# Optimization experiments

Hardware: AMD Instinct MI355X
Metric: run time of the kernel (lower is better)

## Reference

```python
import jax, jax.numpy as jnp
import numpy as np

N, L, M, NNZ, P, G, H = 4096, 64, 256, 100000, 3, 1, 8
D = M // H  # head_dim = 32


def setup_inputs() -> dict:
    key = jax.random.key(0)
    ks = jax.random.split(key, 8)
    return {
        "sparse_values": jax.random.normal(ks[0], (NNZ, M), jnp.float32),
        "linear_index": jax.random.randint(ks[1], (N, L), 0, NNZ, jnp.int32),
        "is_specified": jax.random.randint(ks[2], (N, L), 0, 2, jnp.int32).astype(bool),
        "query": jax.random.normal(ks[3], (N, M), jnp.float32),
        "key_weight": jax.random.normal(ks[4], (M, M), jnp.float32) * 0.05,
        "value_weight": jax.random.normal(ks[5], (M, M), jnp.float32) * 0.05,
        "key_positions": jax.random.uniform(ks[6], (N, L, P), jnp.float32),
        "rope_freqs": jax.random.normal(ks[7], (P, G, H, D // 2), jnp.float32),
        "n_heads": H,
    }


def reference(sparse_values, linear_index, is_specified, query, key_weight,
              value_weight, key_positions, rope_freqs, n_heads):
    n, l = linear_index.shape
    m = query.shape[-1]
    h = n_heads
    d = m // h
    scale = 1.0 / np.sqrt(m)  # docstring: default scale_factor = 1/sqrt(M)

    # Gather each query's key subset; unspecified keys -> 0 (will be masked)
    safe_idx = jnp.where(is_specified, linear_index, 0)
    gathered = jnp.where(is_specified[..., None], sparse_values[safe_idx], 0.0)  # [N,L,M]

    # Key / value projections (nn.Linear convention: x @ W.T)
    k = (gathered @ key_weight.T).reshape(n, l, h, d)
    v = (gathered @ value_weight.T).reshape(n, l, h, d)

    # RoPE on keys: angles [N,L,H,D/2], summed over position dims P and freq groups G
    angles = jnp.einsum('nlp,pghd->nlhd', key_positions, rope_freqs)
    cos, sin = jnp.cos(angles), jnp.sin(angles)
    k_even, k_odd = k[..., 0::2], k[..., 1::2]
    k = jnp.stack([k_even * cos - k_odd * sin,
                   k_even * sin + k_odd * cos], axis=-1).reshape(n, l, h, d)

    # Per-query subset attention (query is pre-rotated per docstring)
    q = query.reshape(n, h, d)
    scores = jnp.einsum('nhd,nlhd->nhl', q, k) * scale
    scores = jnp.where(is_specified[:, None, :], scores, -jnp.inf)

    # Queries with all keys unspecified -> zero output (avoid NaN from all -inf)
    any_spec = is_specified.any(axis=-1)  # [N]
    attn = jax.nn.softmax(jnp.where(any_spec[:, None, None], scores, 0.0), axis=-1)
    out = jnp.einsum('nhl,nlhd->nhd', attn, v).reshape(n, m)
    out = jnp.where(any_spec[:, None], out, 0.0)
    return out, is_specified
```

## Files before the change

### kernel.cpp

```cpp
#include <hip/hip_runtime.h>
#include <math.h>

#define N_Q 4096
#define L_K 64
#define M_D 256

typedef float f32x16 __attribute__((ext_vector_type(16)));
typedef __bf16 b16x8 __attribute__((ext_vector_type(8)));
union F8 { uint4 u; unsigned short s[8]; b16x8 v; };

__device__ __forceinline__ unsigned short f2bf(float x) {
  unsigned u = __float_as_uint(x);
  return (unsigned short)((u + 0x7fffu + ((u >> 16) & 1u)) >> 16);
}

__global__ __launch_bounds__(256) void k_prep(const unsigned char* __restrict__ raw,
                                              float* __restrict__ out2,
                                              const float* __restrict__ wv,
                                              float* __restrict__ wvt,
                                              const float* __restrict__ wk,
                                              unsigned short* __restrict__ wkf,
                                              const int* __restrict__ lin,
                                              int* __restrict__ pcnt,
                                              int* __restrict__ plin,
                                              unsigned char* __restrict__ pl) {
  __shared__ int pll_s[256];
  __shared__ unsigned char pls_s[256];
  __shared__ int pc_s[4];
  const int tid = threadIdx.x, lane = tid & 63;
  pll_s[tid] = 0;
  pls_s[tid] = 0;
  int v = 0;
  for (int i = tid; i < 4096; i += 256)
    if (i & 3) v |= raw[i];
  int f = __syncthreads_or(v);
  const int gi = blockIdx.x * 256 + tid;
  bool b = f ? (raw[gi] != 0) : (((const int*)raw)[gi] != 0);
  out2[gi] = b ? 1.0f : 0.0f;
  int li = lin[gi];
  unsigned long long mask = __ballot(b);
  if (b) {
    int rank = __popcll(mask & ((1ull << lane) - 1));
    pll_s[(tid & 192) + rank] = li;
    pls_s[(tid & 192) + rank] = (unsigned char)lane;
  }
  if (lane == 0) pc_s[tid >> 6] = __popcll(mask);
  __syncthreads();
  plin[gi] = pll_s[tid];
  pl[gi] = pls_s[tid];
  if (tid < 4) pcnt[blockIdx.x * 4 + tid] = pc_s[tid];

  if (gi < 65536) {
    wvt[(gi & 255) * 256 + (gi >> 8)] = wv[gi];
    int oc = gi >> 8, k = gi & 255;
    int tt = oc >> 5, c32o = oc & 31;
    int ks = k >> 4, kg2 = (k >> 3) & 1, j = k & 7;
    wkf[(((tt * 16 + ks) << 6) + kg2 * 32 + c32o) * 8 + j] = f2bf(wk[gi]);
  }
}

#define SC_OFF  32768
#define AT_OFF  (SC_OFF + 2048)
#define LDS_SZ  (AT_OFF + 2048)

__global__ __launch_bounds__(256, 4) void k_fused3(
    const float* __restrict__ sv, const float* __restrict__ q,
    const unsigned short* __restrict__ wkf, const float* __restrict__ pos,
    const float* __restrict__ freqs, const int* __restrict__ pcnt,
    const int* __restrict__ plin, const unsigned char* __restrict__ pl,
    unsigned short* __restrict__ agg) {
  __shared__ __align__(16) char smem[LDS_SZ];
  float* sc_s   = (float*)(smem + SC_OFF);
  float* attn_s = (float*)(smem + AT_OFF);
  const int tid = threadIdx.x, lane = tid & 63, w = tid >> 6;
  const int c32 = lane & 31, kg = lane >> 5;
  const int rt = w >> 1, ch = w & 1;
  const int n = blockIdx.x;
  const int cnt = pcnt[n];

  if (cnt == 0) {
    *(uint4*)((char*)agg + (size_t)n * 4096 + tid * 16) = uint4{0, 0, 0, 0};
    return;
  }
  const int ct32 = (cnt + 31) & ~31;
  const int ntiles = ct32 >> 5;

  {
    const int r0 = tid >> 5, ii = tid & 31;
    #pragma unroll
    for (int pp = 0; pp < 8; ++pp) {
      const int rloc = pp * 8 + r0;
      if (rloc < ct32) {
        const int pe = (rloc < cnt) ? rloc : (cnt - 1);
        const float* rp = sv + (size_t)plin[n * 64 + pe] * 256 + ii * 8;
        float4 f0 = *(const float4*)rp;
        float4 f1 = *(const float4*)(rp + 4);
        F8 pk;
        pk.s[0] = f2bf(f0.x); pk.s[1] = f2bf(f0.y); pk.s[2] = f2bf(f0.z); pk.s[3] = f2bf(f0.w);
        pk.s[4] = f2bf(f1.x); pk.s[5] = f2bf(f1.y); pk.s[6] = f2bf(f1.z); pk.s[7] = f2bf(f1.w);
        *(uint4*)(smem + rloc * 512 + ((ii ^ (rloc & 31)) << 4)) = pk.u;
      }
    }
  }

  const int p = rt * 32 + c32;
  const bool pv = p < cnt;
  const int pe2 = pv ? p : (cnt - 1);
  const int l = pl[n * 64 + pe2];
  const float* lp = pos + ((size_t)n * 64 + l) * 3;
  const float pp0 = lp[0], pp1 = lp[1], pp2 = lp[2];

  __syncthreads();

  if (rt < ntiles) {
    f32x16 acc[4];
    #pragma unroll
    for (int t = 0; t < 4; ++t)
      #pragma unroll
      for (int r = 0; r < 16; ++r) acc[t][r] = 0.0f;

    const char* fbase = (const char*)wkf + ch * 65536 + lane * 16;
    F8 afc[4], afn[4];
    #pragma unroll
    for (int t = 0; t < 4; ++t) afc[t].u = *(const uint4*)(fbase + (t * 16) * 1024);

    #pragma unroll
    for (int ks = 0; ks < 16; ++ks) {
      if (ks < 15) {
        #pragma unroll
        for (int t = 0; t < 4; ++t)
          afn[t].u = *(const uint4*)(fbase + (t * 16 + ks + 1) * 1024);
      }
      F8 bf;
      bf.u = *(const uint4*)(smem + (rt * 32 + c32) * 512 + ((((ks << 1) + kg) ^ c32) << 4));
      #pragma unroll
      for (int t = 0; t < 4; ++t)
        acc[t] = __builtin_amdgcn_mfma_f32_32x32x16_bf16(afc[t].v, bf.v, acc[t], 0, 0, 0);
      #pragma unroll
      for (int t = 0; t < 4; ++t) afc[t] = afn[t];
    }

    #pragma unroll
    for (int t = 0; t < 4; ++t) {
      const int h = ch * 4 + t;
      const float* qh = q + (size_t)n * 256 + h * 32;
      const float* F = freqs + h * 16;
      float s = 0.f;
      #pragma unroll
      for (int g = 0; g < 4; ++g) {
        #pragma unroll
        for (int pr = 0; pr < 2; ++pr) {
          const int d0 = g * 8 + kg * 4 + pr * 2;
          const int jj = d0 >> 1;
          const int r = g * 4 + pr * 2;
          float ke = acc[t][r], ko = acc[t][r + 1];
          float ang = pp0 * F[jj] + pp1 * F[128 + jj] + pp2 * F[256 + jj];
          float sn = __sinf(ang), cs = __cosf(ang);
          float2 qq = *(const float2*)(qh + d0);
          s += ke * (cs * qq.x + sn * qq.y) + ko * (cs * qq.y - sn * qq.x);
        }
      }
      s += __shfl_xor(s, 32);
      if (kg == 0 && pv) sc_s[p * 8 + h] = s * 0.0625f;
    }
  }
  __syncthreads();

  #pragma unroll
  for (int uu = 0; uu < 2; ++uu) {
    const int h = w * 2 + uu;
    const bool vl = lane < cnt;
    float v = vl ? sc_s[lane * 8 + h] : -__builtin_inff();
    float mx = v;
    #pragma unroll
    for (int o = 32; o; o >>= 1) mx = fmaxf(mx, __shfl_xor(mx, o));
    float e = vl ? __expf(v - mx) : 0.f;
    float sm = e;
    #pragma unroll
    for (int o = 32; o; o >>= 1) sm += __shfl_xor(sm, o);
    if (vl) attn_s[lane * 8 + h] = e / sm;
  }
  __syncthreads();

  const int m = tid;
  float ga[8];
  #pragma unroll
  for (int h = 0; h < 8; ++h) ga[h] = 0.f;
  #pragma unroll 4
  for (int p2 = 0; p2 < cnt; ++p2) {
    unsigned short us = *(const unsigned short*)(smem + p2 * 512 +
                        ((((m >> 3) ^ (p2 & 31)) << 4) | ((m & 7) << 1)));
    float gv = __uint_as_float((unsigned)us << 16);
    const float4* ap = (const float4*)(attn_s + p2 * 8);
    float4 aA = ap[0], aB = ap[1];
    ga[0] += aA.x * gv; ga[1] += aA.y * gv; ga[2] += aA.z * gv; ga[3] += aA.w * gv;
    ga[4] += aB.x * gv; ga[5] += aB.y * gv; ga[6] += aB.z * gv; ga[7] += aB.w * gv;
  }
  #pragma unroll
  for (int h = 0; h < 8; ++h)
    agg[(size_t)n * 2048 + h * 256 + m] = f2bf(ga[h]);
}

__global__ __launch_bounds__(256) void k_out(const unsigned short* __restrict__ agg,
                                             const float* __restrict__ wvt,
                                             float* __restrict__ out) {
  __shared__ float a_s[4][8][260];
  const int tid = threadIdx.x;
  const int n0 = blockIdx.x * 4;
  #pragma unroll
  for (int it = 0; it < 4; ++it) {
    uint4 v = *(const uint4*)(agg + (size_t)(n0 + it) * 2048 + tid * 8);
    const unsigned short* sp = (const unsigned short*)&v;
    const int hh = tid >> 5, m0 = (tid & 31) * 8;
    #pragma unroll
    for (int k2 = 0; k2 < 8; ++k2)
      a_s[it][hh][m0 + k2] = __uint_as_float((unsigned)sp[k2] << 16);
  }
  __syncthreads();
  const int m = tid, h = m >> 5;
  float o0 = 0.f, o1 = 0.f, o2 = 0.f, o3 = 0.f;
  #pragma unroll 8
  for (int j = 0; j < 256; ++j) {
    float wvv = wvt[j * 256 + m];
    o0 += a_s[0][h][j] * wvv;
    o1 += a_s[1][h][j] * wvv;
    o2 += a_s[2][h][j] * wvv;
    o3 += a_s[3][h][j] * wvv;
  }
  out[(n0 + 0) * 256 + m] = o0;
  out[(n0 + 1) * 256 + m] = o1;
  out[(n0 + 2) * 256 + m] = o2;
  out[(n0 + 3) * 256 + m] = o3;
}

extern "C" void kernel_launch(void* const* d_in, const int* in_sizes, int n_in,
                              void* d_out, int out_size, void* d_ws, size_t ws_size,
                              hipStream_t stream) {
  const float* sv  = (const float*)d_in[0];
  const int* lin   = (const int*)d_in[1];
  const unsigned char* raw = (const unsigned char*)d_in[2];
  const float* q   = (const float*)d_in[3];
  const float* wk  = (const float*)d_in[4];
  const float* wv  = (const float*)d_in[5];
  const float* pos = (const float*)d_in[6];
  const float* fq  = (const float*)d_in[7];
  float* out = (float*)d_out;
  char* ws = (char*)d_ws;

  float* wvt          = (float*)ws;
  unsigned short* wkf = (unsigned short*)(ws + 262144);
  int* pcnt           = (int*)(ws + 393216);
  int* plin           = (int*)(ws + 409600);
  unsigned char* pl   = (unsigned char*)(ws + 1458176);
  unsigned short* agg = (unsigned short*)(ws + 1720320);

  k_prep  <<<1024, 256, 0, stream>>>(raw, out + N_Q * M_D, wv, wvt, wk, wkf,
                                     lin, pcnt, plin, pl);
  k_fused3<<<4096, 256, 0, stream>>>(sv, q, wkf, pos, fq, pcnt, plin, pl, agg);
  k_out   <<<1024, 256, 0, stream>>>(agg, wvt, out);
}
```

Measured before the change: 107.8 us.

## Pre-convert sparse table to bf16 and double-buffer async row gathers into LDS

Adds a kernel that converts the entire sparse_values table to bf16, then gathers rows from that image directly into LDS via global_load_lds. Each block now processes four queries, prefetching the next query's rows into a second LDS buffer while computing the current one, and the XOR swizzle is replaced with a padded row stride. The aim is to hide gather latency and halve gather bytes, at the cost of a full-table conversion pass each call and lower occupancy.

```diff
diff --git a/kernel.cpp b/kernel.cpp
--- a/kernel.cpp
+++ b/kernel.cpp
@@ -4,6 +4,7 @@
 #define N_Q 4096
 #define L_K 64
 #define M_D 256
+#define NNZ_ROWS 100000
 
 typedef float f32x16 __attribute__((ext_vector_type(16)));
 typedef __bf16 b16x8 __attribute__((ext_vector_type(8)));
@@ -12,6 +13,19 @@
 __device__ __forceinline__ unsigned short f2bf(float x) {
   unsigned u = __float_as_uint(x);
   return (unsigned short)((u + 0x7fffu + ((u >> 16) & 1u)) >> 16);
+}
+
+__global__ __launch_bounds__(256) void k_img(const float* __restrict__ sv,
+                                             unsigned short* __restrict__ img) {
+  const int s = blockIdx.x * 256 + threadIdx.x;
+  const int r = s >> 5, k0 = (s & 31) << 3;
+  const float* rp = sv + (size_t)r * 256 + k0;
+  float4 f0 = *(const float4*)rp;
+  float4 f1 = *(const float4*)(rp + 4);
+  F8 pk;
+  pk.s[0] = f2bf(f0.x); pk.s[1] = f2bf(f0.y); pk.s[2] = f2bf(f0.z); pk.s[3] = f2bf(f0.w);
+  pk.s[4] = f2bf(f1.x); pk.s[5] = f2bf(f1.y); pk.s[6] = f2bf(f1.z); pk.s[7] = f2bf(f1.w);
+  *(uint4*)(img + (size_t)r * 256 + k0) = pk.u;
 }
 
 __global__ __launch_bounds__(256) void k_prep(const unsigned char* __restrict__ raw,
@@ -59,146 +73,155 @@
   }
 }
 
-#define SC_OFF  32768
-#define AT_OFF  (SC_OFF + 2048)
-#define LDS_SZ  (AT_OFF + 2048)
-
-__global__ __launch_bounds__(256, 4) void k_fused3(
-    const float* __restrict__ sv, const float* __restrict__ q,
+#define GSTRIDE 560
+#define BUF_SZ  (64 * GSTRIDE)
+#define SC_OFF  (2 * BUF_SZ)
+#define LDS_SZ  (SC_OFF + 2048)
+
+__global__ __launch_bounds__(256, 2) void k_fused5(
+    const unsigned short* __restrict__ img, const float* __restrict__ q,
     const unsigned short* __restrict__ wkf, const float* __restrict__ pos,
     const float* __restrict__ freqs, const int* __restrict__ pcnt,
     const int* __restrict__ plin, const unsigned char* __restrict__ pl,
     unsigned short* __restrict__ agg) {
   __shared__ __align__(16) char smem[LDS_SZ];
-  float* sc_s   = (float*)(smem + SC_OFF);
-  float* attn_s = (float*)(smem + AT_OFF);
+  float* sc_s = (float*)(smem + SC_OFF);
   const int tid = threadIdx.x, lane = tid & 63, w = tid >> 6;
   const int c32 = lane & 31, kg = lane >> 5;
   const int rt = w >> 1, ch = w & 1;
-  const int n = blockIdx.x;
-  const int cnt = pcnt[n];
-
-  if (cnt == 0) {
-    *(uint4*)((char*)agg + (size_t)n * 4096 + tid * 16) = uint4{0, 0, 0, 0};
-    return;
-  }
-  const int ct32 = (cnt + 31) & ~31;
-  const int ntiles = ct32 >> 5;
-
-  {
-    const int r0 = tid >> 5, ii = tid & 31;
-    #pragma unroll
-    for (int pp = 0; pp < 8; ++pp) {
-      const int rloc = pp * 8 + r0;
-      if (rloc < ct32) {
-        const int pe = (rloc < cnt) ? rloc : (cnt - 1);
-        const float* rp = sv + (size_t)plin[n * 64 + pe] * 256 + ii * 8;
-        float4 f0 = *(const float4*)rp;
-        float4 f1 = *(const float4*)(rp + 4);
-        F8 pk;
-        pk.s[0] = f2bf(f0.x); pk.s[1] = f2bf(f0.y); pk.s[2] = f2bf(f0.z); pk.s[3] = f2bf(f0.w);
-        pk.s[4] = f2bf(f1.x); pk.s[5] = f2bf(f1.y); pk.s[6] = f2bf(f1.z); pk.s[7] = f2bf(f1.w);
-        *(uint4*)(smem + rloc * 512 + ((ii ^ (rloc & 31)) << 4)) = pk.u;
+  const int n_base = blockIdx.x * 4;
+
+  auto stage = [&](int n, char* buf, int cn) {
+    #pragma unroll
+    for (int j = 0; j < 16; ++j) {
+      const int r = w * 16 + j;
+      if (r < cn) {
+        const int pv = plin[n * 64 + r];
+        const unsigned int* src =
+            (const unsigned int*)((const char*)img + (size_t)pv * 512);
+        __builtin_amdgcn_global_load_lds(
+            (const __attribute__((address_space(1))) unsigned int*)(src + lane),
+            (__attribute__((address_space(3))) unsigned int*)(buf + r * GSTRIDE), 4, 0, 0);
+        __builtin_amdgcn_global_load_lds(
+            (const __attribute__((address_space(1))) unsigned int*)(src + 64 + lane),
+            (__attribute__((address_space(3))) unsigned int*)(buf + r * GSTRIDE + 256), 4, 0, 0);
       }
     }
-  }
-
-  const int p = rt * 32 + c32;
-  const bool pv = p < cnt;
-  const int pe2 = pv ? p : (cnt - 1);
-  const int l = pl[n * 64 + pe2];
-  const float* lp = pos + ((size_t)n * 64 + l) * 3;
-  const float pp0 = lp[0], pp1 = lp[1], pp2 = lp[2];
-
+  };
+
+  char* gcur = smem;
+  char* gnxt = smem + BUF_SZ;
+  int cn_cur = pcnt[n_base];
+  stage(n_base, gcur, cn_cur);
+  asm volatile("s_waitcnt vmcnt(0)" ::: "memory");
   __syncthreads();
 
-  if (rt < ntiles) {
-    f32x16 acc[4];
-    #pragma unroll
-    for (int t = 0; t < 4; ++t)
-      #pragma unroll
-      for (int r = 0; r < 16; ++r) acc[t][r] = 0.0f;
-
-    const char* fbase = (const char*)wkf + ch * 65536 + lane * 16;
-    F8 afc[4], afn[4];
-    #pragma unroll
-    for (int t = 0; t < 4; ++t) afc[t].u = *(const uint4*)(fbase + (t * 16) * 1024);
-
-    #pragma unroll
-    for (int ks = 0; ks < 16; ++ks) {
-      if (ks < 15) {
+  #pragma unroll
+  for (int it = 0; it < 4; ++it) {
+    const int n = n_base + it;
+    const int cn_next = (it < 3) ? pcnt[n + 1] : 0;
+    if (it < 3) stage(n + 1, gnxt, cn_next);
+
+    const int ntiles = (cn_cur + 31) >> 5;
+
+    if (rt < ntiles) {
+      f32x16 acc[4];
+      #pragma unroll
+      for (int t = 0; t < 4; ++t)
+        #pragma unroll
+        for (int r = 0; r < 16; ++r) acc[t][r] = 0.0f;
+
+      const char* fbase = (const char*)wkf + ch * 65536 + lane * 16;
+      F8 afc[4], afn[4];
+      #pragma unroll
+      for (int t = 0; t < 4; ++t) afc[t].u = *(const uint4*)(fbase + (t * 16) * 1024);
+
+      #pragma unroll
+      for (int ks = 0; ks < 16; ++ks) {
+        if (ks < 15) {
+          #pragma unroll
+          for (int t = 0; t < 4; ++t)
+            afn[t].u = *(const uint4*)(fbase + (t * 16 + ks + 1) * 1024);
+        }
+        F8 bf;
+        bf.u = *(const uint4*)(gcur + (rt * 32 + c32) * GSTRIDE + ((ks << 1) + kg) * 16);
         #pragma unroll
         for (int t = 0; t < 4; ++t)
-          afn[t].u = *(const uint4*)(fbase + (t * 16 + ks + 1) * 1024);
+          acc[t] = __builtin_amdgcn_mfma_f32_32x32x16_bf16(afc[t].v, bf.v, acc[t], 0, 0, 0);
+        #pragma unroll
+        for (int t = 0; t < 4; ++t) afc[t] = afn[t];
       }
-      F8 bf;
-      bf.u = *(const uint4*)(smem + (rt * 32 + c32) * 512 + ((((ks << 1) + kg) ^ c32) << 4));
-      #pragma unroll
-      for (int t = 0; t < 4; ++t)
-        acc[t] = __builtin_amdgcn_mfma_f32_32x32x16_bf16(afc[t].v, bf.v, acc[t], 0, 0, 0);
-      #pragma unroll
-      for (int t = 0; t < 4; ++t) afc[t] = afn[t];
-    }
-
-    #pragma unroll
-    for (int t = 0; t < 4; ++t) {
-      const int h = ch * 4 + t;
-      const float* qh = q + (size_t)n * 256 + h * 32;
-      const float* F = freqs + h * 16;
-      float s = 0.f;
-      #pragma unroll
-      for (int g = 0; g < 4; ++g) {
-        #pragma unroll
-        for (int pr = 0; pr < 2; ++pr) {
-          const int d0 = g * 8 + kg * 4 + pr * 2;
-          const int jj = d0 >> 1;
-          const int r = g * 4 + pr * 2;
-          float ke = acc[t][r], ko = acc[t][r + 1];
-          float ang = pp0 * F[jj] + pp1 * F[128 + jj] + pp2 * F[256 + jj];
-          float sn = __sinf(ang), cs = __cosf(ang);
-          float2 qq = *(const float2*)(qh + d0);
-          s += ke * (cs * qq.x + sn * qq.y) + ko * (cs * qq.y - sn * qq.x);
+
+      const int p = rt * 32 + c32;
+      const bool pv = p < cn_cur;
+      const int pe2 = pv ? p : (cn_cur > 0 ? cn_cur - 1 : 0);
+      const int l = pl[n * 64 + pe2];
+      const float* lp = pos + ((size_t)n * 64 + l) * 3;
+      const float pp0 = lp[0], pp1 = lp[1], pp2 = lp[2];
+      #pragma unroll
+      for (int t = 0; t < 4; ++t) {
+        const int h = ch * 4 + t;
+        const float* qh = q + (size_t)n * 256 + h * 32;
+        const float* F = freqs + h * 16;
+        float s = 0.f;
+        #pragma unroll
+        for (int g = 0; g < 4; ++g) {
+          #pragma unroll
+          for (int pr = 0; pr < 2; ++pr) {
+            const int d0 = g * 8 + kg * 4 + pr * 2;
+            const int jj = d0 >> 1;
+            const int r = g * 4 + pr * 2;
+            float ke = acc[t][r], ko = acc[t][r + 1];
+            float ang = pp0 * F[jj] + pp1 * F[128 + jj] + pp2 * F[256 + jj];
+            float sn = __sinf(ang), cs = __cosf(ang);
+            float2 qq = *(const float2*)(qh + d0);
+            s += ke * (cs * qq.x + sn * qq.y) + ko * (cs * qq.y - sn * qq.x);
+          }
         }
+        s += __shfl_xor(s, 32);
+        if (kg == 0 && pv) sc_s[p * 8 + h] = s * 0.0625f;
       }
-      s += __shfl_xor(s, 32);
-      if (kg == 0 && pv) sc_s[p * 8 + h] = s * 0.0625f;
-    }
-  }
-  __syncthreads();
-
-  #pragma unroll
-  for (int uu = 0; uu < 2; ++uu) {
-    const int h = w * 2 + uu;
-    const bool vl = lane < cnt;
-    float v = vl ? sc_s[lane * 8 + h] : -__builtin_inff();
-    float mx = v;
-    #pragma unroll
-    for (int o = 32; o; o >>= 1) mx = fmaxf(mx, __shfl_xor(mx, o));
-    float e = vl ? __expf(v - mx) : 0.f;
-    float sm = e;
-    #pragma unroll
-    for (int o = 32; o; o >>= 1) sm += __shfl_xor(sm, o);
-    if (vl) attn_s[lane * 8 + h] = e / sm;
-  }
-  __syncthreads();
-
-  const int m = tid;
-  float ga[8];
-  #pragma unroll
-  for (int h = 0; h < 8; ++h) ga[h] = 0.f;
-  #pragma unroll 4
-  for (int p2 = 0; p2 < cnt; ++p2) {
-    unsigned short us = *(const unsigned short*)(smem + p2 * 512 +
-                        ((((m >> 3) ^ (p2 & 31)) << 4) | ((m & 7) << 1)));
-    float gv = __uint_as_float((unsigned)us << 16);
-    const float4* ap = (const float4*)(attn_s + p2 * 8);
-    float4 aA = ap[0], aB = ap[1];
-    ga[0] += aA.x * gv; ga[1] += aA.y * gv; ga[2] += aA.z * gv; ga[3] += aA.w * gv;
-    ga[4] += aB.x * gv; ga[5] += aB.y * gv; ga[6] += aB.z * gv; ga[7] += aB.w * gv;
-  }
-  #pragma unroll
-  for (int h = 0; h < 8; ++h)
-    agg[(size_t)n * 2048 + h * 256 + m] = f2bf(ga[h]);
+    }
+    __syncthreads();
+
+    #pragma unroll
+    for (int uu = 0; uu < 2; ++uu) {
+      const int h = w * 2 + uu;
+      const bool vl = lane < cn_cur;
+      float v = vl ? sc_s[lane * 8 + h] : -__builtin_inff();
+      float mx = v;
+      #pragma unroll
+      for (int o = 32; o; o >>= 1) mx = fmaxf(mx, __shfl_xor(mx, o));
+      float e = vl ? __expf(v - mx) : 0.f;
+      float sm = e;
+      #pragma unroll
+      for (int o = 32; o; o >>= 1) sm += __shfl_xor(sm, o);
+      if (vl) sc_s[lane * 8 + h] = e / sm;
+    }
+    __syncthreads();
+
+    const int m = tid;
+    float ga[8];
+    #pragma unroll
+    for (int h = 0; h < 8; ++h) ga[h] = 0.f;
+    #pragma unroll 4
+    for (int p2 = 0; p2 < cn_cur; ++p2) {
+      unsigned short us = *(const unsigned short*)(gcur + p2 * GSTRIDE + m * 2);
+      float gv = __uint_as_float((unsigned)us << 16);
+      const float4* ap = (const float4*)(sc_s + p2 * 8);
+      float4 aA = ap[0], aB = ap[1];
+      ga[0] += aA.x * gv; ga[1] += aA.y * gv; ga[2] += aA.z * gv; ga[3] += aA.w * gv;
+      ga[4] += aB.x * gv; ga[5] += aB.y * gv; ga[6] += aB.z * gv; ga[7] += aB.w * gv;
+    }
+    #pragma unroll
+    for (int h = 0; h < 8; ++h)
+      agg[(size_t)n * 2048 + h * 256 + m] = f2bf(ga[h]);
+
+    asm volatile("s_waitcnt vmcnt(0)" ::: "memory");
+    __syncthreads();
+    char* tpp = gcur; gcur = gnxt; gnxt = tpp;
+    cn_cur = cn_next;
+  }
 }
 
 __global__ __launch_bounds__(256) void k_out(const unsigned short* __restrict__ agg,
@@ -253,9 +276,11 @@
   int* plin           = (int*)(ws + 409600);
   unsigned char* pl   = (unsigned char*)(ws + 1458176);
   unsigned short* agg = (unsigned short*)(ws + 1720320);
-
+  unsigned short* img = (unsigned short*)(ws + 18497536);
+
+  k_img   <<<12500, 256, 0, stream>>>(sv, img);
   k_prep  <<<1024, 256, 0, stream>>>(raw, out + N_Q * M_D, wv, wvt, wk, wkf,
                                      lin, pcnt, plin, pl);
-  k_fused3<<<4096, 256, 0, stream>>>(sv, q, wkf, pos, fq, pcnt, plin, pl, agg);
+  k_fused5<<<1024, 256, 0, stream>>>(img, q, wkf, pos, fq, pcnt, plin, pl, agg);
   k_out   <<<1024, 256, 0, stream>>>(agg, wvt, out);
 }
```

Measured after the change: 169.9 us. 57.6% more time.

## Widen fused attention block to 1024 threads with one head per wave

Applied to the files above, without the earlier changes.

The fused kernel now launches 1024-thread blocks. Each of 16 waves owns one head and one 32-row key tile, so a wave runs a single MFMA accumulator chain instead of four. The softmax uses 8 waves, and the weighted aggregation splits the heads across 4 thread groups with two heads each. The aim is more parallelism per query and less register pressure per wave. The cost is that the B fragments are read from LDS repeatedly across heads, and about half the waves sit idle when there are 32 or fewer valid keys.

```diff
diff --git a/kernel.cpp b/kernel.cpp
--- a/kernel.cpp
+++ b/kernel.cpp
@@ -63,7 +63,7 @@
 #define AT_OFF  (SC_OFF + 2048)
 #define LDS_SZ  (AT_OFF + 2048)
 
-__global__ __launch_bounds__(256, 4) void k_fused3(
+__global__ __launch_bounds__(1024, 8) void k_fused6(
     const float* __restrict__ sv, const float* __restrict__ q,
     const unsigned short* __restrict__ wkf, const float* __restrict__ pos,
     const float* __restrict__ freqs, const int* __restrict__ pcnt,
@@ -74,23 +74,24 @@
   float* attn_s = (float*)(smem + AT_OFF);
   const int tid = threadIdx.x, lane = tid & 63, w = tid >> 6;
   const int c32 = lane & 31, kg = lane >> 5;
-  const int rt = w >> 1, ch = w & 1;
+  const int hd = w & 7, rt = w >> 3;
   const int n = blockIdx.x;
   const int cnt = pcnt[n];
 
   if (cnt == 0) {
-    *(uint4*)((char*)agg + (size_t)n * 4096 + tid * 16) = uint4{0, 0, 0, 0};
+    if (tid < 512)
+      *(uint4*)((char*)agg + (size_t)n * 4096 + tid * 8) = uint4{0, 0, 0, 0};
     return;
   }
-  const int ct32 = (cnt + 31) & ~31;
-  const int ntiles = ct32 >> 5;
+  const int ntiles = (cnt + 31) >> 5;
+  const int nrows = ntiles << 5;
 
   {
     const int r0 = tid >> 5, ii = tid & 31;
     #pragma unroll
-    for (int pp = 0; pp < 8; ++pp) {
-      const int rloc = pp * 8 + r0;
-      if (rloc < ct32) {
+    for (int pp = 0; pp < 2; ++pp) {
+      const int rloc = pp * 32 + r0;
+      if (rloc < nrows) {
         const int pe = (rloc < cnt) ? rloc : (cnt - 1);
         const float* rp = sv + (size_t)plin[n * 64 + pe] * 256 + ii * 8;
         float4 f0 = *(const float4*)rp;
@@ -103,9 +104,9 @@
     }
   }
 
-  const int p = rt * 32 + c32;
-  const bool pv = p < cnt;
-  const int pe2 = pv ? p : (cnt - 1);
+  const int p = (rt << 5) + c32;
+  const bool pv = (rt < ntiles) && (p < cnt);
+  const int pe2 = pv ? p : 0;
   const int l = pl[n * 64 + pe2];
   const float* lp = pos + ((size_t)n * 64 + l) * 3;
   const float pp0 = lp[0], pp1 = lp[1], pp2 = lp[2];
@@ -113,64 +114,47 @@
   __syncthreads();
 
   if (rt < ntiles) {
-    f32x16 acc[4];
-    #pragma unroll
-    for (int t = 0; t < 4; ++t)
+    f32x16 acc;
+    #pragma unroll
+    for (int r = 0; r < 16; ++r) acc[r] = 0.0f;
+
+    const char* fb = (const char*)wkf + (hd << 14) + lane * 16;
+    F8 afc, afn;
+    afc.u = *(const uint4*)fb;
+    #pragma unroll
+    for (int ks = 0; ks < 16; ++ks) {
+      if (ks < 15) afn.u = *(const uint4*)(fb + (ks + 1) * 1024);
+      F8 bf;
+      bf.u = *(const uint4*)(smem + ((rt << 5) + c32) * 512 + ((((ks << 1) + kg) ^ c32) << 4));
+      acc = __builtin_amdgcn_mfma_f32_32x32x16_bf16(afc.v, bf.v, acc, 0, 0, 0);
+      afc = afn;
+    }
+
+    const float* qh = q + (size_t)n * 256 + hd * 32;
+    const float* F = freqs + hd * 16;
+    float s = 0.f;
+    #pragma unroll
+    for (int g = 0; g < 4; ++g) {
       #pragma unroll
-      for (int r = 0; r < 16; ++r) acc[t][r] = 0.0f;
-
-    const char* fbase = (const char*)wkf + ch * 65536 + lane * 16;
-    F8 afc[4], afn[4];
-    #pragma unroll
-    for (int t = 0; t < 4; ++t) afc[t].u = *(const uint4*)(fbase + (t * 16) * 1024);
-
-    #pragma unroll
-    for (int ks = 0; ks < 16; ++ks) {
-      if (ks < 15) {
-        #pragma unroll
-        for (int t = 0; t < 4; ++t)
-          afn[t].u = *(const uint4*)(fbase + (t * 16 + ks + 1) * 1024);
+      for (int pr = 0; pr < 2; ++pr) {
+        const int d0 = g * 8 + kg * 4 + pr * 2;
+        const int jj = d0 >> 1;
+        const int r = g * 4 + pr * 2;
+        float ke = acc[r], ko = acc[r + 1];
+        float ang = pp0 * F[jj] + pp1 * F[128 + jj] + pp2 * F[256 + jj];
+        float sn = __sinf(ang), cs = __cosf(ang);
+        float2 qq = *(const float2*)(qh + d0);
+        s += ke * (cs * qq.x + sn * qq.y) + ko * (cs * qq.y - sn * qq.x);
       }
-      F8 bf;
-      bf.u = *(const uint4*)(smem + (rt * 32 + c32) * 512 + ((((ks << 1) + kg) ^ c32) << 4));
-      #pragma unroll
-      for (int t = 0; t < 4; ++t)
-        acc[t] = __builtin_amdgcn_mfma_f32_32x32x16_bf16(afc[t].v, bf.v, acc[t], 0, 0, 0);
-      #pragma unroll
-      for (int t = 0; t < 4; ++t) afc[t] = afn[t];
     }
-
-    #pragma unroll
-    for (int t = 0; t < 4; ++t) {
-      const int h = ch * 4 + t;
-      const float* qh = q + (size_t)n * 256 + h * 32;
-      const float* F = freqs + h * 16;
-      float s = 0.f;
-      #pragma unroll
-      for (int g = 0; g < 4; ++g) {
-        #pragma unroll
-        for (int pr = 0; pr < 2; ++pr) {
-          const int d0 = g * 8 + kg * 4 + pr * 2;
-          const int jj = d0 >> 1;
-          const int r = g * 4 + pr * 2;
-          float ke = acc[t][r], ko = acc[t][r + 1];
-          float ang = pp0 * F[jj] + pp1 * F[128 + jj] + pp2 * F[256 + jj];
-          float sn = __sinf(ang), cs = __cosf(ang);
-          float2 qq = *(const float2*)(qh + d0);
-          s += ke * (cs * qq.x + sn * qq.y) + ko * (cs * qq.y - sn * qq.x);
-        }
-      }
-      s += __shfl_xor(s, 32);
-      if (kg == 0 && pv) sc_s[p * 8 + h] = s * 0.0625f;
-    }
-  }
-  __syncthreads();
-
-  #pragma unroll
-  for (int uu = 0; uu < 2; ++uu) {
-    const int h = w * 2 + uu;
+    s += __shfl_xor(s, 32);
+    if (kg == 0 && pv) sc_s[p * 8 + hd] = s * 0.0625f;
+  }
+  __syncthreads();
+
+  if (w < 8) {
     const bool vl = lane < cnt;
-    float v = vl ? sc_s[lane * 8 + h] : -__builtin_inff();
+    float v = vl ? sc_s[lane * 8 + w] : -__builtin_inff();
     float mx = v;
     #pragma unroll
     for (int o = 32; o; o >>= 1) mx = fmaxf(mx, __shfl_xor(mx, o));
@@ -178,27 +162,23 @@
     float sm = e;
     #pragma unroll
     for (int o = 32; o; o >>= 1) sm += __shfl_xor(sm, o);
-    if (vl) attn_s[lane * 8 + h] = e / sm;
-  }
-  __syncthreads();
-
-  const int m = tid;
-  float ga[8];
-  #pragma unroll
-  for (int h = 0; h < 8; ++h) ga[h] = 0.f;
+    if (vl) attn_s[lane * 8 + w] = e / sm;
+  }
+  __syncthreads();
+
+  const int m = tid & 255, hh = tid >> 8;
+  float g0 = 0.f, g1 = 0.f;
   #pragma unroll 4
   for (int p2 = 0; p2 < cnt; ++p2) {
     unsigned short us = *(const unsigned short*)(smem + p2 * 512 +
                         ((((m >> 3) ^ (p2 & 31)) << 4) | ((m & 7) << 1)));
     float gv = __uint_as_float((unsigned)us << 16);
-    const float4* ap = (const float4*)(attn_s + p2 * 8);
-    float4 aA = ap[0], aB = ap[1];
-    ga[0] += aA.x * gv; ga[1] += aA.y * gv; ga[2] += aA.z * gv; ga[3] += aA.w * gv;
-    ga[4] += aB.x * gv; ga[5] += aB.y * gv; ga[6] += aB.z * gv; ga[7] += aB.w * gv;
-  }
-  #pragma unroll
-  for (int h = 0; h < 8; ++h)
-    agg[(size_t)n * 2048 + h * 256 + m] = f2bf(ga[h]);
+    float2 a = *(const float2*)(attn_s + p2 * 8 + hh * 2);
+    g0 += a.x * gv;
+    g1 += a.y * gv;
+  }
+  agg[(size_t)n * 2048 + (hh * 2) * 256 + m]     = f2bf(g0);
+  agg[(size_t)n * 2048 + (hh * 2 + 1) * 256 + m] = f2bf(g1);
 }
 
 __global__ __launch_bounds__(256) void k_out(const unsigned short* __restrict__ agg,
@@ -256,6 +236,6 @@
 
   k_prep  <<<1024, 256, 0, stream>>>(raw, out + N_Q * M_D, wv, wvt, wk, wkf,
                                      lin, pcnt, plin, pl);
-  k_fused3<<<4096, 256, 0, stream>>>(sv, q, wkf, pos, fq, pcnt, plin, pl, agg);
+  k_fused6<<<4096, 1024, 0, stream>>>(sv, q, wkf, pos, fq, pcnt, plin, pl, agg);
   k_out   <<<1024, 256, 0, stream>>>(agg, wvt, out);
 }
```

Result: slower. 120.0 us (+11.4%).

## Batch gather loads, stage query and freqs in LDS, raise MFMA priority

Applied to the files above, without the earlier changes.

The fused kernel now loads all eight gather row pointers up front with one plin load per lane broadcast by shuffle. It issues the sparse-row loads in two batches of four behind a sched barrier so more global loads are in flight. Query and RoPE frequencies are staged in shared memory instead of being read from global inside the score loop, the MFMA loop runs at raised wave priority, and the aggregation loop unroll goes from 4 to 8. It costs more registers and LDS per block, and rows beyond the valid count are now loaded unconditionally even though they are not stored.

```diff
diff --git a/kernel.cpp b/kernel.cpp
--- a/kernel.cpp
+++ b/kernel.cpp
@@ -61,9 +61,11 @@
 
 #define SC_OFF  32768
 #define AT_OFF  (SC_OFF + 2048)
-#define LDS_SZ  (AT_OFF + 2048)
-
-__global__ __launch_bounds__(256, 4) void k_fused3(
+#define Q_OFF   (AT_OFF + 2048)
+#define FR_OFF  (Q_OFF + 1024)
+#define LDS_SZ  (FR_OFF + 1536)
+
+__global__ __launch_bounds__(256, 4) void k_fused8(
     const float* __restrict__ sv, const float* __restrict__ q,
     const unsigned short* __restrict__ wkf, const float* __restrict__ pos,
     const float* __restrict__ freqs, const int* __restrict__ pcnt,
@@ -72,6 +74,8 @@
   __shared__ __align__(16) char smem[LDS_SZ];
   float* sc_s   = (float*)(smem + SC_OFF);
   float* attn_s = (float*)(smem + AT_OFF);
+  float* q_s    = (float*)(smem + Q_OFF);
+  float* fr_s   = (float*)(smem + FR_OFF);
   const int tid = threadIdx.x, lane = tid & 63, w = tid >> 6;
   const int c32 = lane & 31, kg = lane >> 5;
   const int rt = w >> 1, ch = w & 1;
@@ -85,20 +89,39 @@
   const int ct32 = (cnt + 31) & ~31;
   const int ntiles = ct32 >> 5;
 
+  q_s[tid] = q[(size_t)n * 256 + tid];
+  for (int i = tid; i < 384; i += 256) fr_s[i] = freqs[i];
+
   {
     const int r0 = tid >> 5, ii = tid & 31;
+    const int myplin = plin[n * 64 + lane];
+    const float* rp[8];
     #pragma unroll
     for (int pp = 0; pp < 8; ++pp) {
       const int rloc = pp * 8 + r0;
-      if (rloc < ct32) {
-        const int pe = (rloc < cnt) ? rloc : (cnt - 1);
-        const float* rp = sv + (size_t)plin[n * 64 + pe] * 256 + ii * 8;
-        float4 f0 = *(const float4*)rp;
-        float4 f1 = *(const float4*)(rp + 4);
-        F8 pk;
-        pk.s[0] = f2bf(f0.x); pk.s[1] = f2bf(f0.y); pk.s[2] = f2bf(f0.z); pk.s[3] = f2bf(f0.w);
-        pk.s[4] = f2bf(f1.x); pk.s[5] = f2bf(f1.y); pk.s[6] = f2bf(f1.z); pk.s[7] = f2bf(f1.w);
-        *(uint4*)(smem + rloc * 512 + ((ii ^ (rloc & 31)) << 4)) = pk.u;
+      const int pe = (rloc < cnt) ? rloc : (cnt - 1);
+      rp[pp] = sv + (size_t)__shfl(myplin, pe) * 256 + ii * 8;
+    }
+    #pragma unroll
+    for (int b = 0; b < 2; ++b) {
+      float4 fa[8];
+      #pragma unroll
+      for (int pp = 0; pp < 4; ++pp) {
+        fa[pp * 2]     = *(const float4*)(rp[b * 4 + pp]);
+        fa[pp * 2 + 1] = *(const float4*)(rp[b * 4 + pp] + 4);
+      }
+      __builtin_amdgcn_sched_barrier(0);
+      #pragma unroll
+      for (int pp = 0; pp < 4; ++pp) {
+        const int rloc = (b * 4 + pp) * 8 + r0;
+        if (rloc < ct32) {
+          F8 pk;
+          pk.s[0] = f2bf(fa[pp * 2].x);     pk.s[1] = f2bf(fa[pp * 2].y);
+          pk.s[2] = f2bf(fa[pp * 2].z);     pk.s[3] = f2bf(fa[pp * 2].w);
+          pk.s[4] = f2bf(fa[pp * 2 + 1].x); pk.s[5] = f2bf(fa[pp * 2 + 1].y);
+          pk.s[6] = f2bf(fa[pp * 2 + 1].z); pk.s[7] = f2bf(fa[pp * 2 + 1].w);
+          *(uint4*)(smem + rloc * 512 + ((ii ^ (rloc & 31)) << 4)) = pk.u;
+        }
       }
     }
   }
@@ -124,6 +147,7 @@
     #pragma unroll
     for (int t = 0; t < 4; ++t) afc[t].u = *(const uint4*)(fbase + (t * 16) * 1024);
 
+    __builtin_amdgcn_s_setprio(1);
     #pragma unroll
     for (int ks = 0; ks < 16; ++ks) {
       if (ks < 15) {
@@ -139,12 +163,13 @@
       #pragma unroll
       for (int t = 0; t < 4; ++t) afc[t] = afn[t];
     }
+    __builtin_amdgcn_s_setprio(0);
 
     #pragma unroll
     for (int t = 0; t < 4; ++t) {
       const int h = ch * 4 + t;
-      const float* qh = q + (size_t)n * 256 + h * 32;
-      const float* F = freqs + h * 16;
+      const float* qh = q_s + h * 32;
+      const float* F = fr_s + h * 16;
       float s = 0.f;
       #pragma unroll
       for (int g = 0; g < 4; ++g) {
@@ -186,7 +211,7 @@
   float ga[8];
   #pragma unroll
   for (int h = 0; h < 8; ++h) ga[h] = 0.f;
-  #pragma unroll 4
+  #pragma unroll 8
   for (int p2 = 0; p2 < cnt; ++p2) {
     unsigned short us = *(const unsigned short*)(smem + p2 * 512 +
                         ((((m >> 3) ^ (p2 & 31)) << 4) | ((m & 7) << 1)));
@@ -256,6 +281,6 @@
 
   k_prep  <<<1024, 256, 0, stream>>>(raw, out + N_Q * M_D, wv, wvt, wk, wkf,
                                      lin, pcnt, plin, pl);
-  k_fused3<<<4096, 256, 0, stream>>>(sv, q, wkf, pos, fq, pcnt, plin, pl, agg);
+  k_fused8<<<4096, 256, 0, stream>>>(sv, q, wkf, pos, fq, pcnt, plin, pl, agg);
   k_out   <<<1024, 256, 0, stream>>>(agg, wvt, out);
 }
```

Result: no change. 105.7 us (-1.9%).
